# Performance work log

Measured on AMD Instinct MI355X. Metric: run time of the kernel, lower is better.

## Reference

```python
import jax, jax.numpy as jnp
import numpy as np

E, H, KVH, S, N = 2048, 16, 4, 4096, 1
D = E // H            # head_dim = 128
G = H // KVH          # groups = 4
KV_DIM = KVH * D


def setup_inputs() -> dict:
    key = jax.random.key(0)
    ks = jax.random.split(key, 7)
    sc = 0.02
    seq = jax.random.normal(ks[0], (N, S, E), dtype=jnp.float32)
    # causal mask, 0 = masked (matches masked_fill(mask == 0, -inf))
    mask = jnp.tril(jnp.ones((S, S), dtype=jnp.int32))[None, None]  # [1,1,S,S]
    return {
        "seq": seq,
        "mask": mask,
        "Wq_w": jax.random.normal(ks[1], (E, E), dtype=jnp.float32) * sc,
        "Wq_b": jnp.zeros((E,), dtype=jnp.float32),
        "Wkv_w": jax.random.normal(ks[2], (2 * KV_DIM, E), dtype=jnp.float32) * sc,
        "Wkv_b": jnp.zeros((2 * KV_DIM,), dtype=jnp.float32),
        "Wo_w": jax.random.normal(ks[3], (E, E), dtype=jnp.float32) * sc,
        "Wo_b": jnp.zeros((E,), dtype=jnp.float32),
    }


def reference(seq, mask, Wq_w, Wq_b, Wkv_w, Wkv_b, Wo_w, Wo_b):
    n, s, _ = seq.shape
    q = seq @ Wq_w.T + Wq_b                      # [N,S,E]
    kv = seq @ Wkv_w.T + Wkv_b                   # [N,S,2*KV_DIM]
    Q = q.reshape(n, s, H, D).transpose(0, 2, 1, 3)         # [N,H,S,D]
    KV = kv.reshape(n, s, 2, KVH, D)
    K = KV[:, :, 0].transpose(0, 2, 1, 3)                   # [N,KVH,S,D]
    V = KV[:, :, 1].transpose(0, 2, 1, 3)                   # [N,KVH,S,D]
    # repeat_interleave over head dim (GQA expansion)
    Kr = jnp.repeat(K, G, axis=1)                           # [N,H,S,D]
    Vr = jnp.repeat(V, G, axis=1)
    energy = jnp.einsum("nhqd,nhkd->nhqk", Q, Kr)           # [N,H,S,S]
    neg = jnp.finfo(energy.dtype).min
    energy = jnp.where(mask == 0, neg, energy)
    attn = jax.nn.softmax(energy / jnp.sqrt(jnp.float32(D)), axis=3)
    out = jnp.einsum("nhqk,nhkd->nhqd", attn, Vr)           # [N,H,S,D]
    out = out.transpose(0, 2, 1, 3).reshape(n, s, E)
    out = out @ Wo_w.T + Wo_b
    return out, K, V
```

## Files before the change

### kernel.cpp

```cpp
#include <hip/hip_runtime.h>
#include <cstdint>
#include <cstddef>

typedef __bf16 bf16_t;
typedef __bf16 bf16x4 __attribute__((ext_vector_type(4)));
typedef __bf16 bf16x8 __attribute__((ext_vector_type(8)));
typedef float  f32x4  __attribute__((ext_vector_type(4)));

#define LDQ 3072

__global__ __launch_bounds__(256)
void cast_kernel(const float* __restrict__ in, bf16_t* __restrict__ out, int n8) {
  int i = blockIdx.x * 256 + threadIdx.x;
  if (i >= n8) return;
  const float4* p = reinterpret_cast<const float4*>(in) + (size_t)i * 2;
  float4 a = p[0], b = p[1];
  bf16x8 o;
  o[0] = (bf16_t)a.x; o[1] = (bf16_t)a.y; o[2] = (bf16_t)a.z; o[3] = (bf16_t)a.w;
  o[4] = (bf16_t)b.x; o[5] = (bf16_t)b.y; o[6] = (bf16_t)b.z; o[7] = (bf16_t)b.w;
  *reinterpret_cast<bf16x8*>(out + (size_t)i * 8) = o;
}

template <int MODE>
__global__ __launch_bounds__(256, 3)
void gemm128(const bf16_t* __restrict__ A, const bf16_t* __restrict__ B,
             const float* __restrict__ bias0, const float* __restrict__ bias1,
             void* __restrict__ out0, float* __restrict__ kvout,
             bf16_t* __restrict__ vt, int M, int N, int K) {
  __shared__ __align__(16) char smem[32768];
  const int t = threadIdx.x;
  const int l = t & 63;
  const int lr = l & 15, lh = l >> 4;
  const int w = t >> 6;
  const int wm = w >> 1, wn = w & 1;
  const int m0 = blockIdx.x * 128, n0 = blockIdx.y * 128;

  const char* Ag = (const char*)(A + (size_t)m0 * K);
  const char* Bg = (const char*)(B + (size_t)n0 * K);

#define STAGE_U(dst, src, ks)                                                   \
  { _Pragma("unroll")                                                           \
    for (int p = 0; p < 2; ++p) {                                               \
      int c = p * 256 + t;                                                      \
      int row = c >> 2;                                                         \
      int c16 = (c & 3) ^ ((row >> 1) & 3);                                     \
      __builtin_amdgcn_global_load_lds(                                         \
        (const __attribute__((address_space(1))) void*)                         \
          ((src) + (size_t)row * (size_t)(K * 2) + (size_t)(ks) * 64 + c16 * 16), \
        (__attribute__((address_space(3))) void*)((dst) + c * 16), 16, 0, 0);   \
    } }

  f32x4 acc[4][4] = {};
  bf16x8 a[4], b[4];
  char* const s0 = smem;
  char* const s1 = smem + 16384;

#define RD_B(base)                                                              \
  { _Pragma("unroll")                                                           \
    for (int j = 0; j < 4; ++j) {                                               \
      int row = wn * 64 + j * 16 + lr;                                          \
      b[j] = *reinterpret_cast<const bf16x8*>(                                  \
          (base) + 8192 + row * 64 + ((lh ^ ((row >> 1) & 3)) << 4));           \
    } }
#define RD_A2(base, i0)                                                         \
  { _Pragma("unroll")                                                           \
    for (int ii = 0; ii < 2; ++ii) {                                            \
      int row = wm * 64 + ((i0) + ii) * 16 + lr;                                \
      a[(i0) + ii] = *reinterpret_cast<const bf16x8*>(                          \
          (base) + row * 64 + ((lh ^ ((row >> 1) & 3)) << 4));                  \
    } }
#define MFMA8(i0)                                                               \
  asm volatile("s_waitcnt lgkmcnt(0)" ::: "memory");                            \
  __builtin_amdgcn_sched_barrier(0);                                            \
  __builtin_amdgcn_s_setprio(1);                                                \
  { _Pragma("unroll")                                                           \
    for (int ii = 0; ii < 2; ++ii)                                              \
      _Pragma("unroll")                                                         \
      for (int j = 0; j < 4; ++j)                                               \
        acc[(i0) + ii][j] =                                                     \
          __builtin_amdgcn_mfma_f32_16x16x32_bf16(a[(i0)+ii], b[j], acc[(i0)+ii][j], 0, 0, 0); } \
  __builtin_amdgcn_s_setprio(0);                                                \
  __builtin_amdgcn_sched_barrier(0);
#define BAR  __builtin_amdgcn_s_barrier(); __builtin_amdgcn_sched_barrier(0);

  const int NK = K >> 5;
  STAGE_U(s0, Ag, 0);
  STAGE_U(s0 + 8192, Bg, 0);

  for (int it2 = 0; it2 < (NK >> 1); ++it2) {
    const int k1 = 2 * it2 + 1, k2 = 2 * it2 + 2;
    STAGE_U(s1, Ag, k1);
    asm volatile("s_waitcnt vmcnt(2)" ::: "memory");
    BAR;
    RD_B(s0); RD_A2(s0, 0);
    MFMA8(0);
    BAR;
    RD_A2(s0, 2);
    STAGE_U(s1 + 8192, Bg, k1);
    MFMA8(2);
    BAR;
    if (k2 < NK) {
      STAGE_U(s0, Ag, k2);
      asm volatile("s_waitcnt vmcnt(2)" ::: "memory");
    } else {
      asm volatile("s_waitcnt vmcnt(0)" ::: "memory");
    }
    BAR;
    RD_B(s1); RD_A2(s1, 0);
    MFMA8(0);
    BAR;
    RD_A2(s1, 2);
    if (k2 < NK) STAGE_U(s0 + 8192, Bg, k2);
    MFMA8(2);
    BAR;
  }
#undef STAGE_U
#undef RD_A2
#undef RD_B
#undef MFMA8
#undef BAR

  #pragma unroll
  for (int j = 0; j < 4; ++j) {
    const int col = n0 + wn * 64 + j * 16 + lr;
    float bv;
    if constexpr (MODE == 0) bv = bias0[col];
    else bv = (col < 2048) ? bias0[col] : bias1[col - 2048];
    #pragma unroll
    for (int i = 0; i < 4; ++i) {
      #pragma unroll
      for (int r = 0; r < 4; ++r) {
        const int row = m0 + wm * 64 + i * 16 + lh * 4 + r;
        float v = acc[i][j][r] + bv;
        if constexpr (MODE == 0) {
          reinterpret_cast<float*>(out0)[(size_t)row * N + col] = v;
        } else {
          float qv = (col < 2048) ? v * 0.1275187541f : v;
          reinterpret_cast<bf16_t*>(out0)[(size_t)row * N + col] = (bf16_t)qv;
          if (col >= 2048) {
            const int local = col - 2048;
            const int which = local >> 9;
            const int hd    = local & 511;
            kvout[(size_t)which * 2097152 +
                  ((size_t)(hd >> 7) * 4096 + row) * 128 + (hd & 127)] = v;
            if (local >= 512) {
              const int c2 = local - 512;
              vt[(size_t)(c2 >> 7) * 524288 + (size_t)(c2 & 127) * 4096 + row] = (bf16_t)v;
            }
          }
        }
      }
    }
  }
}

__global__ __launch_bounds__(256, 2)
void attn_kernel(const bf16_t* __restrict__ QKVb, const bf16_t* __restrict__ Vt,
                 bf16_t* __restrict__ Ob) {
  __shared__ __align__(16) char smem[65536];
  const int t = threadIdx.x;
  const int w = t >> 6, l = t & 63;
  const int lr = l & 15, lh = l >> 4;
  const int g = w >> 1;
  const int wq = w & 1;
  const int h = blockIdx.y, kvh = h >> 2;

  const char* Kg = (const char*)(QKVb + 2048 + (size_t)kvh * 128);
  const char* Vg = (const char*)(Vt + (size_t)kvh * 524288);

#define STAGE_K(buf, kv0)                                                          \
  {                                                                                \
    _Pragma("unroll")                                                              \
    for (int p = 0; p < 4; ++p) {                                                  \
      int chunk = p * 256 + t;                                                     \
      int row = chunk >> 4, cb = (chunk & 15) << 4;                                \
      __builtin_amdgcn_global_load_lds(                                            \
        (const __attribute__((address_space(1))) void*)                            \
            (Kg + (size_t)((kv0) + row) * 6144 + (cb ^ ((row & 7) << 4))),         \
        (__attribute__((address_space(3))) void*)(smem + (buf) * 16384 + chunk * 16),\
        16, 0, 0);                                                                 \
    }                                                                              \
  }
#define STAGE_V(buf, kv0)                                                          \
  {                                                                                \
    _Pragma("unroll")                                                              \
    for (int p = 0; p < 4; ++p) {                                                  \
      int chunk = p * 256 + t;                                                     \
      int row = chunk >> 3, cb = (chunk & 7) << 4;                                 \
      __builtin_amdgcn_global_load_lds(                                            \
        (const __attribute__((address_space(1))) void*)                            \
            (Vg + (size_t)row * 8192 + (size_t)(kv0) * 2 + (cb ^ ((row & 7) << 4))),\
        (__attribute__((address_space(3))) void*)(smem + 32768 + (buf) * 16384 + chunk * 16),\
        16, 0, 0);                                                                 \
    }                                                                              \
  }

  bf16x8 onesf;
  #pragma unroll
  for (int j = 0; j < 8; ++j) onesf[j] = (bf16_t)1.0f;

  for (int ph = 0; ph < 2; ++ph) {
    const int xt = ph ? 63 - (int)blockIdx.x : (int)blockIdx.x;
    const int q0b = xt * 64;
    const int q0w = q0b + wq * 32;
    const int nIter = xt + 1;

    bf16x8 qf[2][4];
    #pragma unroll
    for (int sub = 0; sub < 2; ++sub) {
      const bf16_t* qp = QKVb + (size_t)(q0w + sub * 16 + lr) * LDQ + h * 128 + lh * 8;
      #pragma unroll
      for (int kc = 0; kc < 4; ++kc) qf[sub][kc] = *reinterpret_cast<const bf16x8*>(qp + kc * 32);
    }
    __builtin_amdgcn_sched_barrier(0);
    STAGE_K(0, 0);
    STAGE_V(0, 0);
    __builtin_amdgcn_sched_barrier(0);
    STAGE_K(1, 64);
    STAGE_V(1, 64);
    __builtin_amdgcn_sched_barrier(0);

    f32x4 oacc[2][8] = {};
    f32x4 lacc[2] = {};

    auto body = [&](int it, bool masked) {
      const int cur = it & 1;
      const int kv0 = it * 64;
      if (it + 1 < nIter) { asm volatile("s_waitcnt vmcnt(8)" ::: "memory"); }
      else                { asm volatile("s_waitcnt vmcnt(0)" ::: "memory"); }
      __builtin_amdgcn_s_barrier();
      __builtin_amdgcn_sched_barrier(0);

      const char* kb = smem + cur * 16384;
      f32x4 s[2][2] = {};
      __builtin_amdgcn_s_setprio(1);
      #pragma unroll
      for (int n2 = 0; n2 < 2; ++n2) {
        const int row = g * 32 + n2 * 16 + lr;
        const int sw = (row & 7) << 4;
        #pragma unroll
        for (int kc = 0; kc < 4; ++kc) {
          bf16x8 kf = *reinterpret_cast<const bf16x8*>(kb + row * 256 + ((kc * 64 + lh * 16) ^ sw));
          s[0][n2] = __builtin_amdgcn_mfma_f32_16x16x32_bf16(kf, qf[0][kc], s[0][n2], 0, 0, 0);
          s[1][n2] = __builtin_amdgcn_mfma_f32_16x16x32_bf16(kf, qf[1][kc], s[1][n2], 0, 0, 0);
        }
      }
      __builtin_amdgcn_s_setprio(0);

      bf16x8 pa[2];
      #pragma unroll
      for (int sub = 0; sub < 2; ++sub) {
        const int qs = q0w + sub * 16;
        const bool needM = masked && (kv0 + g * 32 + 31 > qs);
        bf16x8 v;
        #pragma unroll
        for (int n2 = 0; n2 < 2; ++n2) {
          #pragma unroll
          for (int r = 0; r < 4; ++r) {
            float p = exp2f(s[sub][n2][r]);
            if (needM && (kv0 + g * 32 + n2 * 16 + lh * 4 + r > qs + lr)) p = 0.f;
            v[n2 * 4 + r] = (bf16_t)p;
          }
        }
        pa[sub] = v;
      }
      lacc[0] = __builtin_amdgcn_mfma_f32_16x16x32_bf16(pa[0], onesf, lacc[0], 0, 0, 0);
      lacc[1] = __builtin_amdgcn_mfma_f32_16x16x32_bf16(pa[1], onesf, lacc[1], 0, 0, 0);

      const char* vb0 = smem + 32768 + cur * 16384;
      __builtin_amdgcn_s_setprio(1);
      #pragma unroll
      for (int nb = 0; nb < 8; ++nb) {
        const int row = nb * 16 + lr;
        const int sw2 = (row & 7) << 4;
        const char* vb = vb0 + row * 128;
        bf16x4 lo = *reinterpret_cast<const bf16x4*>(vb + ((g * 64 + lh * 8) ^ sw2));
        bf16x4 hi = *reinterpret_cast<const bf16x4*>(vb + ((g * 64 + 32 + lh * 8) ^ sw2));
        bf16x8 vf = __builtin_shufflevector(lo, hi, 0, 1, 2, 3, 4, 5, 6, 7);
        oacc[0][nb] = __builtin_amdgcn_mfma_f32_16x16x32_bf16(pa[0], vf, oacc[0][nb], 0, 0, 0);
        oacc[1][nb] = __builtin_amdgcn_mfma_f32_16x16x32_bf16(pa[1], vf, oacc[1][nb], 0, 0, 0);
      }
      __builtin_amdgcn_s_setprio(0);

      __builtin_amdgcn_sched_barrier(0);
      __builtin_amdgcn_s_barrier();
      __builtin_amdgcn_sched_barrier(0);
      if (it + 2 < nIter) { STAGE_K(cur, kv0 + 128); STAGE_V(cur, kv0 + 128); }
    };

    for (int it = 0; it < nIter - 1; ++it) body(it, false);
    body(nIter - 1, true);

    bf16_t* mO = (bf16_t*)smem;
    float*  mL = (float*)(smem + 32768);
    if (g == 1) {
      #pragma unroll
      for (int sub = 0; sub < 2; ++sub) {
        #pragma unroll
        for (int nb = 0; nb < 8; ++nb)
          #pragma unroll
          for (int r = 0; r < 4; ++r)
            mO[((wq * 32 + sub * 16 + lh * 4 + r) << 7) + nb * 16 + lr] = (bf16_t)oacc[sub][nb][r];
        if (lr == 0)
          #pragma unroll
          for (int r = 0; r < 4; ++r) mL[wq * 32 + sub * 16 + lh * 4 + r] = lacc[sub][r];
      }
    }
    __syncthreads();
    if (g == 0) {
      #pragma unroll
      for (int sub = 0; sub < 2; ++sub) {
        f32x4 linv;
        #pragma unroll
        for (int r = 0; r < 4; ++r)
          linv[r] = 1.0f / (lacc[sub][r] + mL[wq * 32 + sub * 16 + lh * 4 + r]);
        #pragma unroll
        for (int nb = 0; nb < 8; ++nb) {
          #pragma unroll
          for (int r = 0; r < 4; ++r) {
            float o1 = (float)mO[((wq * 32 + sub * 16 + lh * 4 + r) << 7) + nb * 16 + lr];
            float v = (oacc[sub][nb][r] + o1) * linv[r];
            Ob[(size_t)(q0w + sub * 16 + lh * 4 + r) * 2048 + h * 128 + nb * 16 + lr] = (bf16_t)v;
          }
        }
      }
    }
    __syncthreads();
  }
#undef STAGE_K
#undef STAGE_V
}

extern "C" void kernel_launch(void* const* d_in, const int* in_sizes, int n_in,
                              void* d_out, int out_size, void* d_ws, size_t ws_size,
                              hipStream_t stream) {
  const float* seq   = (const float*)d_in[0];
  const float* Wq_w  = (const float*)d_in[2];
  const float* Wq_b  = (const float*)d_in[3];
  const float* Wkv_w = (const float*)d_in[4];
  const float* Wkv_b = (const float*)d_in[5];
  const float* Wo_w  = (const float*)d_in[6];
  const float* Wo_b  = (const float*)d_in[7];

  float* out   = (float*)d_out;
  float* kvout = out + (size_t)4096 * 2048;

  char* ws = (char*)d_ws;
  bf16_t* seqb = (bf16_t*)ws;
  bf16_t* wqkv = (bf16_t*)(ws + 16777216);
  bf16_t* wob  = (bf16_t*)(ws + 29360128);
  bf16_t* qkvb = (bf16_t*)(ws + 37748736);
  bf16_t* vt   = (bf16_t*)(ws + 62914560);
  bf16_t* ob   = seqb;

  cast_kernel<<<4096, 256, 0, stream>>>(seq, seqb, 1048576);
  cast_kernel<<<2048, 256, 0, stream>>>(Wq_w, wqkv, 524288);
  cast_kernel<<<1024, 256, 0, stream>>>(Wkv_w, wqkv + 4194304, 262144);
  cast_kernel<<<2048, 256, 0, stream>>>(Wo_w, wob, 524288);

  gemm128<1><<<dim3(32, 24), 256, 0, stream>>>(seqb, wqkv, Wq_b, Wkv_b,
                                               qkvb, kvout, vt, 4096, 3072, 2048);
  attn_kernel<<<dim3(32, 16), 256, 0, stream>>>(qkvb, vt, ob);
  gemm128<0><<<dim3(32, 16), 256, 0, stream>>>(ob, wob, Wo_b, nullptr,
                                               out, nullptr, nullptr, 4096, 2048, 2048);
}
```

Measured before the change: 225.2 us.

## Switch attention kernel to 32x32x16 MFMA tiles with permlane P repacking

Rewrites the attention inner loop to use 32x32x16 bf16 MFMA instead of 16x16x32, so each wave computes a 32x32 score tile with one accumulator and fewer, larger matrix instructions. The P fragments are packed with v_cvt_pk_bf16_f32 and rearranged across half-waves with v_permlane32_swap, so they can feed the PV MFMA directly without going through LDS. V reads become full 16-byte LDS loads, and the epilogue indexing is adapted to the 32x32 output layout. The aim is to cut instruction count and LDS traffic per tile, at the cost of more fragile lane-layout code.

Result: slower. 231.3 us (+2.7%).

```diff
diff --git a/kernel.cpp b/kernel.cpp
--- a/kernel.cpp
+++ b/kernel.cpp
@@ -3,9 +3,10 @@
 #include <cstddef>
 
 typedef __bf16 bf16_t;
-typedef __bf16 bf16x4 __attribute__((ext_vector_type(4)));
 typedef __bf16 bf16x8 __attribute__((ext_vector_type(8)));
 typedef float  f32x4  __attribute__((ext_vector_type(4)));
+typedef float  f32x16 __attribute__((ext_vector_type(16)));
+typedef unsigned int u32x4 __attribute__((ext_vector_type(4)));
 
 #define LDQ 3072
 
@@ -160,7 +161,7 @@
   __shared__ __align__(16) char smem[65536];
   const int t = threadIdx.x;
   const int w = t >> 6, l = t & 63;
-  const int lr = l & 15, lh = l >> 4;
+  const int q5 = l & 31, hi = l >> 5;
   const int g = w >> 1;
   const int wq = w & 1;
   const int h = blockIdx.y, kvh = h >> 2;
@@ -194,6 +195,7 @@
         16, 0, 0);                                                                 \
     }                                                                              \
   }
+#define CROW(r) (((r) & 3) + 8 * ((r) >> 2) + 4 * hi)
 
   bf16x8 onesf;
   #pragma unroll
@@ -201,16 +203,14 @@
 
   for (int ph = 0; ph < 2; ++ph) {
     const int xt = ph ? 63 - (int)blockIdx.x : (int)blockIdx.x;
-    const int q0b = xt * 64;
-    const int q0w = q0b + wq * 32;
+    const int q0w = xt * 64 + wq * 32;
     const int nIter = xt + 1;
 
-    bf16x8 qf[2][4];
-    #pragma unroll
-    for (int sub = 0; sub < 2; ++sub) {
-      const bf16_t* qp = QKVb + (size_t)(q0w + sub * 16 + lr) * LDQ + h * 128 + lh * 8;
-      #pragma unroll
-      for (int kc = 0; kc < 4; ++kc) qf[sub][kc] = *reinterpret_cast<const bf16x8*>(qp + kc * 32);
+    bf16x8 qf[8];
+    {
+      const bf16_t* qp = QKVb + (size_t)(q0w + q5) * LDQ + h * 128 + hi * 8;
+      #pragma unroll
+      for (int kc = 0; kc < 8; ++kc) qf[kc] = *reinterpret_cast<const bf16x8*>(qp + kc * 16);
     }
     __builtin_amdgcn_sched_barrier(0);
     STAGE_K(0, 0);
@@ -220,8 +220,8 @@
     STAGE_V(1, 64);
     __builtin_amdgcn_sched_barrier(0);
 
-    f32x4 oacc[2][8] = {};
-    f32x4 lacc[2] = {};
+    f32x16 oacc[4] = {};
+    f32x16 lacc = {};
 
     auto body = [&](int it, bool masked) {
       const int cur = it & 1;
@@ -231,54 +231,55 @@
       __builtin_amdgcn_s_barrier();
       __builtin_amdgcn_sched_barrier(0);
 
-      const char* kb = smem + cur * 16384;
-      f32x4 s[2][2] = {};
+      const int krow = g * 32 + q5;
+      const char* ka = smem + cur * 16384 + krow * 256;
+      const int ksw = (krow & 7) << 4;
+      f32x16 s = {};
       __builtin_amdgcn_s_setprio(1);
       #pragma unroll
-      for (int n2 = 0; n2 < 2; ++n2) {
-        const int row = g * 32 + n2 * 16 + lr;
-        const int sw = (row & 7) << 4;
-        #pragma unroll
-        for (int kc = 0; kc < 4; ++kc) {
-          bf16x8 kf = *reinterpret_cast<const bf16x8*>(kb + row * 256 + ((kc * 64 + lh * 16) ^ sw));
-          s[0][n2] = __builtin_amdgcn_mfma_f32_16x16x32_bf16(kf, qf[0][kc], s[0][n2], 0, 0, 0);
-          s[1][n2] = __builtin_amdgcn_mfma_f32_16x16x32_bf16(kf, qf[1][kc], s[1][n2], 0, 0, 0);
-        }
+      for (int kc = 0; kc < 8; ++kc) {
+        bf16x8 kf = *reinterpret_cast<const bf16x8*>(ka + ((kc * 32 + hi * 16) ^ ksw));
+        s = __builtin_amdgcn_mfma_f32_32x32x16_bf16(kf, qf[kc], s, 0, 0, 0);
       }
       __builtin_amdgcn_s_setprio(0);
 
-      bf16x8 pa[2];
-      #pragma unroll
-      for (int sub = 0; sub < 2; ++sub) {
-        const int qs = q0w + sub * 16;
-        const bool needM = masked && (kv0 + g * 32 + 31 > qs);
-        bf16x8 v;
-        #pragma unroll
-        for (int n2 = 0; n2 < 2; ++n2) {
-          #pragma unroll
-          for (int r = 0; r < 4; ++r) {
-            float p = exp2f(s[sub][n2][r]);
-            if (needM && (kv0 + g * 32 + n2 * 16 + lh * 4 + r > qs + lr)) p = 0.f;
-            v[n2 * 4 + r] = (bf16_t)p;
-          }
-        }
-        pa[sub] = v;
-      }
-      lacc[0] = __builtin_amdgcn_mfma_f32_16x16x32_bf16(pa[0], onesf, lacc[0], 0, 0, 0);
-      lacc[1] = __builtin_amdgcn_mfma_f32_16x16x32_bf16(pa[1], onesf, lacc[1], 0, 0, 0);
+      float e_[16];
+      #pragma unroll
+      for (int r = 0; r < 16; ++r) {
+        float p = exp2f(s[r]);
+        if (masked && (kv0 + g * 32 + CROW(r) > q0w + q5)) p = 0.f;
+        e_[r] = p;
+      }
+      unsigned int pk_[8];
+      #pragma unroll
+      for (int pr = 0; pr < 8; ++pr) {
+        unsigned int wrd;
+        asm("v_cvt_pk_bf16_f32 %0, %1, %2" : "=v"(wrd) : "v"(e_[2 * pr]), "v"(e_[2 * pr + 1]));
+        pk_[pr] = wrd;
+      }
+      asm("v_permlane32_swap_b32 %0, %1" : "+v"(pk_[0]), "+v"(pk_[2]));
+      asm("v_permlane32_swap_b32 %0, %1" : "+v"(pk_[1]), "+v"(pk_[3]));
+      asm("v_permlane32_swap_b32 %0, %1" : "+v"(pk_[4]), "+v"(pk_[6]));
+      asm("v_permlane32_swap_b32 %0, %1" : "+v"(pk_[5]), "+v"(pk_[7]));
+      u32x4 pw0 = {pk_[0], pk_[1], pk_[2], pk_[3]};
+      u32x4 pw1 = {pk_[4], pk_[5], pk_[6], pk_[7]};
+      bf16x8 pa0 = *reinterpret_cast<bf16x8*>(&pw0);
+      bf16x8 pa1 = *reinterpret_cast<bf16x8*>(&pw1);
+
+      lacc = __builtin_amdgcn_mfma_f32_32x32x16_bf16(pa0, onesf, lacc, 0, 0, 0);
+      lacc = __builtin_amdgcn_mfma_f32_32x32x16_bf16(pa1, onesf, lacc, 0, 0, 0);
 
       const char* vb0 = smem + 32768 + cur * 16384;
       __builtin_amdgcn_s_setprio(1);
       #pragma unroll
-      for (int nb = 0; nb < 8; ++nb) {
-        const int row = nb * 16 + lr;
-        const int sw2 = (row & 7) << 4;
-        const char* vb = vb0 + row * 128;
-        bf16x4 lo = *reinterpret_cast<const bf16x4*>(vb + ((g * 64 + lh * 8) ^ sw2));
-        bf16x4 hi = *reinterpret_cast<const bf16x4*>(vb + ((g * 64 + 32 + lh * 8) ^ sw2));
-        bf16x8 vf = __builtin_shufflevector(lo, hi, 0, 1, 2, 3, 4, 5, 6, 7);
-        oacc[0][nb] = __builtin_amdgcn_mfma_f32_16x16x32_bf16(pa[0], vf, oacc[0][nb], 0, 0, 0);
-        oacc[1][nb] = __builtin_amdgcn_mfma_f32_16x16x32_bf16(pa[1], vf, oacc[1][nb], 0, 0, 0);
+      for (int db = 0; db < 4; ++db) {
+        const int vrow = db * 32 + q5;
+        const char* va = vb0 + vrow * 128;
+        const int vsw = (vrow & 7) << 4;
+        bf16x8 v0 = *reinterpret_cast<const bf16x8*>(va + ((g * 64 + hi * 16) ^ vsw));
+        bf16x8 v1 = *reinterpret_cast<const bf16x8*>(va + ((g * 64 + 32 + hi * 16) ^ vsw));
+        oacc[db] = __builtin_amdgcn_mfma_f32_32x32x16_bf16(pa0, v0, oacc[db], 0, 0, 0);
+        oacc[db] = __builtin_amdgcn_mfma_f32_32x32x16_bf16(pa1, v1, oacc[db], 0, 0, 0);
       }
       __builtin_amdgcn_s_setprio(0);
 
@@ -295,33 +296,27 @@
     float*  mL = (float*)(smem + 32768);
     if (g == 1) {
       #pragma unroll
-      for (int sub = 0; sub < 2; ++sub) {
+      for (int db = 0; db < 4; ++db)
         #pragma unroll
-        for (int nb = 0; nb < 8; ++nb)
-          #pragma unroll
-          for (int r = 0; r < 4; ++r)
-            mO[((wq * 32 + sub * 16 + lh * 4 + r) << 7) + nb * 16 + lr] = (bf16_t)oacc[sub][nb][r];
-        if (lr == 0)
-          #pragma unroll
-          for (int r = 0; r < 4; ++r) mL[wq * 32 + sub * 16 + lh * 4 + r] = lacc[sub][r];
-      }
+        for (int r = 0; r < 16; ++r)
+          mO[(wq * 32 + CROW(r)) * 128 + db * 32 + q5] = (bf16_t)oacc[db][r];
+      if (q5 == 0)
+        #pragma unroll
+        for (int r = 0; r < 16; ++r) mL[wq * 32 + CROW(r)] = lacc[r];
     }
     __syncthreads();
     if (g == 0) {
-      #pragma unroll
-      for (int sub = 0; sub < 2; ++sub) {
-        f32x4 linv;
+      float linv[16];
+      #pragma unroll
+      for (int r = 0; r < 16; ++r)
+        linv[r] = 1.0f / (lacc[r] + mL[wq * 32 + CROW(r)]);
+      #pragma unroll
+      for (int db = 0; db < 4; ++db) {
         #pragma unroll
-        for (int r = 0; r < 4; ++r)
-          linv[r] = 1.0f / (lacc[sub][r] + mL[wq * 32 + sub * 16 + lh * 4 + r]);
-        #pragma unroll
-        for (int nb = 0; nb < 8; ++nb) {
-          #pragma unroll
-          for (int r = 0; r < 4; ++r) {
-            float o1 = (float)mO[((wq * 32 + sub * 16 + lh * 4 + r) << 7) + nb * 16 + lr];
-            float v = (oacc[sub][nb][r] + o1) * linv[r];
-            Ob[(size_t)(q0w + sub * 16 + lh * 4 + r) * 2048 + h * 128 + nb * 16 + lr] = (bf16_t)v;
-          }
+        for (int r = 0; r < 16; ++r) {
+          float o1 = (float)mO[(wq * 32 + CROW(r)) * 128 + db * 32 + q5];
+          float v = (oacc[db][r] + o1) * linv[r];
+          Ob[(size_t)(q0w + CROW(r)) * 2048 + h * 128 + db * 32 + q5] = (bf16_t)v;
         }
       }
     }
@@ -329,6 +324,7 @@
   }
 #undef STAGE_K
 #undef STAGE_V
+#undef CROW
 }
 
 extern "C" void kernel_launch(void* const* d_in, const int* in_sizes, int n_in,
```

## Load V fragments straight from global into registers, bypassing LDS staging

Applied to the files above, without the earlier changes.

Stops staging the transposed V tile through shared memory with global_load_lds. Each wave now loads its V MFMA fragments directly from global memory into registers, prefetched one iteration ahead, while K stays double-buffered in LDS. This halves shared memory use and removes the LDS reads and part of the LDS traffic for V, and the vmcnt waits are adjusted to match. In exchange, V global reads are duplicated across the two query-wave halves, the loads are narrow 8-byte strided accesses, and the prefetch buffer costs extra registers.

Result: slower. 389.7 us (+73.0%).

```diff
diff --git a/kernel.cpp b/kernel.cpp
--- a/kernel.cpp
+++ b/kernel.cpp
@@ -157,7 +157,7 @@
 __global__ __launch_bounds__(256, 2)
 void attn_kernel(const bf16_t* __restrict__ QKVb, const bf16_t* __restrict__ Vt,
                  bf16_t* __restrict__ Ob) {
-  __shared__ __align__(16) char smem[65536];
+  __shared__ __align__(16) char smem[32768];
   const int t = threadIdx.x;
   const int w = t >> 6, l = t & 63;
   const int lr = l & 15, lh = l >> 4;
@@ -181,17 +181,14 @@
         16, 0, 0);                                                                 \
     }                                                                              \
   }
-#define STAGE_V(buf, kv0)                                                          \
+#define LOADV(valo, vahi, kv0)                                                     \
   {                                                                                \
     _Pragma("unroll")                                                              \
-    for (int p = 0; p < 4; ++p) {                                                  \
-      int chunk = p * 256 + t;                                                     \
-      int row = chunk >> 3, cb = (chunk & 7) << 4;                                 \
-      __builtin_amdgcn_global_load_lds(                                            \
-        (const __attribute__((address_space(1))) void*)                            \
-            (Vg + (size_t)row * 8192 + (size_t)(kv0) * 2 + (cb ^ ((row & 7) << 4))),\
-        (__attribute__((address_space(3))) void*)(smem + 32768 + (buf) * 16384 + chunk * 16),\
-        16, 0, 0);                                                                 \
+    for (int nb = 0; nb < 8; ++nb) {                                               \
+      const char* vr_ = Vg + (size_t)(nb * 16 + lr) * 8192 +                       \
+                        (size_t)((kv0) + g * 32) * 2 + lh * 8;                     \
+      valo[nb] = *reinterpret_cast<const bf16x4*>(vr_);                            \
+      vahi[nb] = *reinterpret_cast<const bf16x4*>(vr_ + 32);                       \
     }                                                                              \
   }
 
@@ -201,8 +198,7 @@
 
   for (int ph = 0; ph < 2; ++ph) {
     const int xt = ph ? 63 - (int)blockIdx.x : (int)blockIdx.x;
-    const int q0b = xt * 64;
-    const int q0w = q0b + wq * 32;
+    const int q0w = xt * 64 + wq * 32;
     const int nIter = xt + 1;
 
     bf16x8 qf[2][4];
@@ -213,11 +209,13 @@
       for (int kc = 0; kc < 4; ++kc) qf[sub][kc] = *reinterpret_cast<const bf16x8*>(qp + kc * 32);
     }
     __builtin_amdgcn_sched_barrier(0);
+
+    bf16x4 valo[8], vahi[8];
     STAGE_K(0, 0);
-    STAGE_V(0, 0);
     __builtin_amdgcn_sched_barrier(0);
-    STAGE_K(1, 64);
-    STAGE_V(1, 64);
+    LOADV(valo, vahi, 0);
+    __builtin_amdgcn_sched_barrier(0);
+    if (nIter > 1) STAGE_K(1, 64);
     __builtin_amdgcn_sched_barrier(0);
 
     f32x4 oacc[2][8] = {};
@@ -226,8 +224,8 @@
     auto body = [&](int it, bool masked) {
       const int cur = it & 1;
       const int kv0 = it * 64;
-      if (it + 1 < nIter) { asm volatile("s_waitcnt vmcnt(8)" ::: "memory"); }
-      else                { asm volatile("s_waitcnt vmcnt(0)" ::: "memory"); }
+      if (it + 1 < nIter) { asm volatile("s_waitcnt vmcnt(20)" ::: "memory"); }
+      else                { asm volatile("s_waitcnt vmcnt(16)" ::: "memory"); }
       __builtin_amdgcn_s_barrier();
       __builtin_amdgcn_sched_barrier(0);
 
@@ -267,16 +265,10 @@
       lacc[0] = __builtin_amdgcn_mfma_f32_16x16x32_bf16(pa[0], onesf, lacc[0], 0, 0, 0);
       lacc[1] = __builtin_amdgcn_mfma_f32_16x16x32_bf16(pa[1], onesf, lacc[1], 0, 0, 0);
 
-      const char* vb0 = smem + 32768 + cur * 16384;
       __builtin_amdgcn_s_setprio(1);
       #pragma unroll
       for (int nb = 0; nb < 8; ++nb) {
-        const int row = nb * 16 + lr;
-        const int sw2 = (row & 7) << 4;
-        const char* vb = vb0 + row * 128;
-        bf16x4 lo = *reinterpret_cast<const bf16x4*>(vb + ((g * 64 + lh * 8) ^ sw2));
-        bf16x4 hi = *reinterpret_cast<const bf16x4*>(vb + ((g * 64 + 32 + lh * 8) ^ sw2));
-        bf16x8 vf = __builtin_shufflevector(lo, hi, 0, 1, 2, 3, 4, 5, 6, 7);
+        bf16x8 vf = __builtin_shufflevector(valo[nb], vahi[nb], 0, 1, 2, 3, 4, 5, 6, 7);
         oacc[0][nb] = __builtin_amdgcn_mfma_f32_16x16x32_bf16(pa[0], vf, oacc[0][nb], 0, 0, 0);
         oacc[1][nb] = __builtin_amdgcn_mfma_f32_16x16x32_bf16(pa[1], vf, oacc[1][nb], 0, 0, 0);
       }
@@ -285,14 +277,17 @@
       __builtin_amdgcn_sched_barrier(0);
       __builtin_amdgcn_s_barrier();
       __builtin_amdgcn_sched_barrier(0);
-      if (it + 2 < nIter) { STAGE_K(cur, kv0 + 128); STAGE_V(cur, kv0 + 128); }
+      if (it + 1 < nIter) LOADV(valo, vahi, kv0 + 64);
+      __builtin_amdgcn_sched_barrier(0);
+      if (it + 2 < nIter) STAGE_K(cur, kv0 + 128);
+      __builtin_amdgcn_sched_barrier(0);
     };
 
     for (int it = 0; it < nIter - 1; ++it) body(it, false);
     body(nIter - 1, true);
 
     bf16_t* mO = (bf16_t*)smem;
-    float*  mL = (float*)(smem + 32768);
+    float*  mL = (float*)(smem + 16384);
     if (g == 1) {
       #pragma unroll
       for (int sub = 0; sub < 2; ++sub) {
@@ -328,7 +323,7 @@
     __syncthreads();
   }
 #undef STAGE_K
-#undef STAGE_V
+#undef LOADV
 }
 
 extern "C" void kernel_launch(void* const* d_in, const int* in_sizes, int n_in,
```
